# Performance work log

Measured on AMD Instinct MI355X. Metric: run time of the kernel, lower is better.

## Reference

```python
import jax, jax.numpy as jnp
import numpy as np
from jax import lax

SQRT2 = float(np.sqrt(2.0))  # lrelu def_gain
LRELU_SLOPE = 0.2


def setup_inputs() -> dict:
    key = jax.random.key(0)
    ks = jax.random.split(key, 4)
    N, I, O, WD, H = 16, 256, 512, 512, 64
    return {
        "x": jax.random.normal(ks[0], (N, I, H, H), dtype=jnp.float32),
        "w": jax.random.normal(ks[1], (N, WD), dtype=jnp.float32),
        "affine_w": jax.random.normal(ks[2], (I, WD), dtype=jnp.float32),
        "affine_b": jnp.ones((I,), dtype=jnp.float32),
        "weight": jax.random.normal(ks[3], (O, I, 3, 3), dtype=jnp.float32),
        "bias": jnp.zeros((O,), dtype=jnp.float32),
    }


def reference(x, w, affine_w, affine_b, weight, bias):
    N, I, H, W = x.shape
    O, _, kh, kw = weight.shape
    w_dim = affine_w.shape[1]

    # affine (FullyConnectedLayer, weight_gain = 1/sqrt(w_dim))
    styles = w @ (affine_w.T / np.sqrt(w_dim)) + affine_b  # [N, I]

    # modulate + demodulate -> per-sample weights [N, O, I, kh, kw]
    ww = weight[None] * styles[:, None, :, None, None]
    dcoefs = lax.rsqrt(jnp.sum(ww * ww, axis=(2, 3, 4)) + 1e-8)  # [N, O]
    ww = ww * dcoefs[:, :, None, None, None]

    # resample filter: outer([1,3,3,1])/sum, symmetric so flip is a no-op
    f1 = jnp.array([1.0, 3.0, 3.0, 1.0], dtype=x.dtype)
    f1 = f1 / f1.sum()
    f2 = jnp.outer(f1, f1)  # [4, 4]

    # upfirdn2d: pad by padding + (fw-down+1)//2 = 2 per side, depthwise 4x4
    xp = jnp.pad(x, ((0, 0), (0, 0), (2, 2), (2, 2)))
    fk = jnp.broadcast_to(f2[None, None], (I, 1, 4, 4))
    xf = lax.conv_general_dilated(
        xp, fk, window_strides=(1, 1), padding="VALID",
        feature_group_count=I,
        dimension_numbers=("NCHW", "OIHW", "NCHW"))  # [N, I, H+1, W+1]

    # fused grouped conv, stride 2; flip_weight=False -> flip kernel spatially
    wk = ww[:, :, :, ::-1, ::-1].reshape(N * O, I, kh, kw)
    xg = xf.reshape(1, N * I, xf.shape[2], xf.shape[3])
    y = lax.conv_general_dilated(
        xg, wk, window_strides=(2, 2), padding="VALID",
        feature_group_count=N,
        dimension_numbers=("NCHW", "OIHW", "NCHW"))
    y = y.reshape(N, O, y.shape[2], y.shape[3])  # [N, O, H/2, W/2]

    # bias + lrelu, act_gain = sqrt(2), no clamp
    y = y + bias[None, :, None, None]
    y = jnp.where(y >= 0, y, LRELU_SLOPE * y) * SQRT2
    return y
```

## Files before the change

### kernel.cpp

```cpp
#include <hip/hip_runtime.h>
#include <cstdint>
#include <cstddef>


typedef short bf16x8 __attribute__((ext_vector_type(8)));
typedef float f32x4  __attribute__((ext_vector_type(4)));

#define CGSTR 4460544
#define NSTR  278784
#define PLSTR 69696

__device__ __forceinline__ unsigned short f2bf(float f) {
  union { float f; unsigned u; } v; v.f = f;
  unsigned r = (v.u + 0x7FFFu + ((v.u >> 16) & 1u)) >> 16;
  return (unsigned short)r;
}

__device__ __forceinline__ void gload_lds16(const void* g, void* l) {
  __builtin_amdgcn_global_load_lds((const __attribute__((address_space(1))) void*)g,
                                   (__attribute__((address_space(3))) void*)l,
                                   16, 0, 0);
}

__global__ void styles_kernel(const float* __restrict__ w, const float* __restrict__ aw,
                              const float* __restrict__ ab, float* __restrict__ styles) {
  const int n = blockIdx.x;
  const int i = threadIdx.x;
  const float4* wr = (const float4*)(w + (size_t)n * 512);
  const float4* ar = (const float4*)(aw + (size_t)i * 512);
  float acc = 0.f;
#pragma unroll 4
  for (int k = 0; k < 128; ++k) {
    float4 a = wr[k], c = ar[k];
    acc += a.x * c.x + a.y * c.y + a.z * c.z + a.w * c.w;
  }
  styles[n * 256 + i] = acc * 0.04419417382415922f + ab[i];
}

__global__ void wtcvt_kernel(const float* __restrict__ wt, unsigned short* __restrict__ wtb,
                             float* __restrict__ wsq) {
  const int o = blockIdx.x;
  const int i = threadIdx.x;
  const float* p = wt + ((size_t)o * 256 + i) * 9;
  float v[9];
  float s = 0.f;
#pragma unroll
  for (int k = 0; k < 9; ++k) { v[k] = p[k]; s += v[k] * v[k]; }
  wsq[o * 256 + i] = s;
#pragma unroll
  for (int tap = 0; tap < 9; ++tap)
    wtb[((size_t)tap * 512 + o) * 256 + i] = f2bf(v[8 - tap]);
}

__global__ void dcoefs_kernel(const float* __restrict__ wsq, const float* __restrict__ styles,
                              float* __restrict__ dcoefs) {
  __shared__ float st2[256];
  const int n = blockIdx.x;
  const int t = threadIdx.x;
  if (t < 256) { float s = styles[n * 256 + t]; st2[t] = s * s; }
  __syncthreads();
  const float4* wr = (const float4*)(wsq + (size_t)t * 256);
  const float4* sr = (const float4*)st2;
  float acc = 0.f;
#pragma unroll 4
  for (int k = 0; k < 64; ++k) {
    float4 a = wr[k], c = sr[k];
    acc += a.x * c.x + a.y * c.y + a.z * c.z + a.w * c.w;
  }
  dcoefs[n * 512 + t] = 1.0f / sqrtf(acc + 1e-8f);
}

__global__ __launch_bounds__(256, 4) void blur_kernel(const float* __restrict__ x,
                                                      const float* __restrict__ styles,
                                                      unsigned short* __restrict__ xfp) {
  __shared__ unsigned short shls[2][64][68];
  const int b = blockIdx.x;
  const int n = b >> 6;
  const int rem = b & 63;
  const int rg = rem >> 2;
  const int cg = rem & 3;
  const int tid = threadIdx.x;
  const int ch = tid >> 2;
  const int s4 = tid & 3;
  const int col0 = s4 * 16;
  const float* xin = x + ((size_t)(n * 256 + cg * 64 + ch) << 12);
  const float sv = styles[n * 256 + cg * 64 + ch];
  const float F0s = 0.125f * sv, F1s = 0.375f * sv;
  const float F0 = 0.125f, F1 = 0.375f;
  const int ybase = rg * 4;
  const int ylim = (rg == 15) ? 5 : 4;
  const size_t obase = (size_t)(cg * 16 + n) * 4 * PLSTR;

  float4 rA[4], rB[4], rC[4], rD[4], rN[4];
  auto load4 = [&](int row, float4* dst) {
    if ((unsigned)row < 64u) {
      const float4* p = (const float4*)(xin + row * 64 + col0);
      dst[0] = p[0]; dst[1] = p[1]; dst[2] = p[2]; dst[3] = p[3];
    } else {
      const float4 z = {0.f, 0.f, 0.f, 0.f};
      dst[0] = z; dst[1] = z; dst[2] = z; dst[3] = z;
    }
  };
  load4(ybase - 2, rA); load4(ybase - 1, rB); load4(ybase, rC); load4(ybase + 1, rD);

#pragma unroll 1
  for (int yy = 0; yy < ylim; ++yy) {
    const int y = ybase + yy;
    load4(y + 2, rN);
    float ve[20];
#pragma unroll
    for (int q = 0; q < 4; ++q) {
      ve[2 + q * 4 + 0] = F0s * rA[q].x + F1s * rB[q].x + F1s * rC[q].x + F0s * rD[q].x;
      ve[2 + q * 4 + 1] = F0s * rA[q].y + F1s * rB[q].y + F1s * rC[q].y + F0s * rD[q].y;
      ve[2 + q * 4 + 2] = F0s * rA[q].z + F1s * rB[q].z + F1s * rC[q].z + F0s * rD[q].z;
      ve[2 + q * 4 + 3] = F0s * rA[q].w + F1s * rB[q].w + F1s * rC[q].w + F0s * rD[q].w;
    }
    float vm2 = __shfl_up(ve[16], 1);
    float vm1 = __shfl_up(ve[17], 1);
    float vp1 = __shfl_down(ve[2], 1);
    if (s4 == 0) { vm2 = 0.f; vm1 = 0.f; }
    if (s4 == 3) vp1 = 0.f;
    ve[0] = vm2; ve[1] = vm1; ve[18] = vp1; ve[19] = 0.f;
    unsigned short hv[17];
#pragma unroll
    for (int pl = 0; pl < 17; ++pl)
      hv[pl] = f2bf(F0 * ve[pl] + F1 * ve[pl + 1] + F1 * ve[pl + 2] + F0 * ve[pl + 3]);
    unsigned short (*sh)[68] = shls[yy & 1];
    unsigned* dst32 = (unsigned*)&sh[ch][col0];
#pragma unroll
    for (int q = 0; q < 8; ++q)
      dst32[q] = (unsigned)hv[2 * q] | ((unsigned)hv[2 * q + 1] << 16);
    if (s4 == 3) sh[ch][64] = hv[16];
    __syncthreads();
    const int ph = y & 1, r = y >> 1;
#pragma unroll 1
    for (int sI = tid; sI < 520; sI += 256) {
      const int p = sI >> 3, j = sI & 7;
      union { bf16x8 vv; unsigned short u[8]; } pk;
#pragma unroll
      for (int k = 0; k < 8; ++k) pk.u[k] = sh[j * 8 + k][p];
      const int pw = p & 1, cc = p >> 1;
      const size_t off = obase + (size_t)(ph * 2 + pw) * PLSTR + (r * 33 + cc) * 64 + j * 8;
      *(bf16x8*)(xfp + off) = pk.vv;
    }
#pragma unroll
    for (int q = 0; q < 4; ++q) { rA[q] = rB[q]; rB[q] = rC[q]; rC[q] = rD[q]; rD[q] = rN[q]; }
  }
}

__global__ __launch_bounds__(256) void conv_kernel(
    const unsigned short* __restrict__ wtb,
    const unsigned short* __restrict__ xfp,
    const float* __restrict__ dcoefs,
    const float* __restrict__ bias,
    float* __restrict__ out) {
  __shared__ unsigned short As0[4096], As1[4096];
  __shared__ unsigned short Bs0[4096], Bs1[4096];
  const int idx = blockIdx.x;
  const int om = idx >> 7;
  const int g = idx & 127;
  const int pt = g >> 4;
  const int n = g & 15;
  const int o0 = om << 7;
  const int oh0 = pt << 2;
  const int tid = threadIdx.x;
  const int lane = tid & 63;
  const int wv = tid >> 6;
  const int wm = wv >> 1;
  const int wp = wv & 1;
  const int ml = lane & 15;
  const int kq = lane >> 4;

  f32x4 acc[4][4];
  const f32x4 zz = {0.f, 0.f, 0.f, 0.f};
#pragma unroll
  for (int i = 0; i < 4; ++i)
#pragma unroll
    for (int j = 0; j < 4; ++j) acc[i][j] = zz;

  const int s0 = wv * 128 + lane, s1 = s0 + 64;
  const int r0 = s0 >> 2, g0 = (s0 & 3) * 8;
  const int r1 = s1 >> 2, g1 = (s1 & 3) * 8;
  const int aoff0 = (o0 + r0) * 256 + g0;
  const int aoff1 = (o0 + r1) * 256 + g1;
  const int row0 = oh0 + (r0 >> 5), col0 = r0 & 31;
  const int row1 = oh0 + (r1 >> 5), col1 = r1 & 31;
  const size_t nB = (size_t)n * NSTR;

  auto stage = [&](int kt, unsigned short* As, unsigned short* Bs) {
    const int tap = kt >> 3, kb = kt & 7;
    const int kh = (tap * 11) >> 5;
    const int kw = tap - kh * 3;
    const int ph = kh & 1, dr = kh >> 1;
    const int pw = kw & 1, dc = kw >> 1;
    const unsigned short* At = wtb + tap * 131072 + kb * 32;
    gload_lds16(At + aoff0, As + wv * 1024);
    gload_lds16(At + aoff1, As + wv * 1024 + 512);
    const unsigned short* Bt = xfp + (size_t)(kb >> 1) * CGSTR + nB +
                               (size_t)(ph * 2 + pw) * PLSTR + (kb & 1) * 32;
    gload_lds16(Bt + ((row0 + dr) * 33 + col0 + dc) * 64 + g0, Bs + wv * 1024);
    gload_lds16(Bt + ((row1 + dr) * 33 + col1 + dc) * 64 + g1, Bs + wv * 1024 + 512);
  };
  auto compute = [&](const unsigned short* As, const unsigned short* Bs) {
    bf16x8 af[4], bfv[4];
    const bf16x8* A8 = (const bf16x8*)As;
    const bf16x8* B8 = (const bf16x8*)Bs;
#pragma unroll
    for (int t = 0; t < 4; ++t) {
      af[t]  = A8[(wm * 64 + t * 16 + ml) * 4 + kq];
      bfv[t] = B8[(wp * 64 + t * 16 + ml) * 4 + kq];
    }
#pragma unroll
    for (int mt = 0; mt < 4; ++mt)
#pragma unroll
      for (int nt = 0; nt < 4; ++nt)
        acc[mt][nt] = __builtin_amdgcn_mfma_f32_16x16x32_bf16(af[mt], bfv[nt], acc[mt][nt], 0, 0, 0);
  };

  stage(0, As0, Bs0);
#pragma unroll 1
  for (int kt = 0; kt < 72; kt += 2) {
    __syncthreads();
    stage(kt + 1, As1, Bs1);
    compute(As0, Bs0);
    __syncthreads();
    if (kt + 2 < 72) stage(kt + 2, As0, Bs0);
    compute(As1, Bs1);
  }

  f32x4 dc4[4], bi4[4];
#pragma unroll
  for (int mt = 0; mt < 4; ++mt) {
    const int ob = o0 + wm * 64 + mt * 16 + kq * 4;
    dc4[mt] = *(const f32x4*)(dcoefs + n * 512 + ob);
    bi4[mt] = *(const f32x4*)(bias + ob);
  }
#pragma unroll
  for (int mt = 0; mt < 4; ++mt) {
#pragma unroll
    for (int nt = 0; nt < 4; ++nt) {
      const int p = wp * 64 + nt * 16 + ml;
      const int oh = oh0 + (p >> 5), ow = p & 31;
#pragma unroll
      for (int r = 0; r < 4; ++r) {
        const int o = o0 + wm * 64 + mt * 16 + kq * 4 + r;
        float v = acc[mt][nt][r] * dc4[mt][r] + bi4[mt][r];
        v = (v >= 0.f ? v : 0.2f * v) * 1.41421356237309515f;
        out[(((size_t)n * 512 + o) * 32 + oh) * 32 + ow] = v;
      }
    }
  }
}

extern "C" void kernel_launch(void* const* d_in, const int* in_sizes, int n_in,
                              void* d_out, int out_size, void* d_ws, size_t ws_size,
                              hipStream_t stream) {
  const float* x  = (const float*)d_in[0];
  const float* w  = (const float*)d_in[1];
  const float* aw = (const float*)d_in[2];
  const float* ab = (const float*)d_in[3];
  const float* wt = (const float*)d_in[4];
  const float* bs = (const float*)d_in[5];
  float* out = (float*)d_out;

  char* ws = (char*)d_ws;
  float* styles        = (float*)(ws);
  float* dcoefs        = (float*)(ws + 16384);
  float* wsq           = (float*)(ws + 49152);
  unsigned short* wtb  = (unsigned short*)(ws + 573440);
  unsigned short* xfp  = (unsigned short*)(ws + 2932736);

  styles_kernel<<<dim3(16),   dim3(256), 0, stream>>>(w, aw, ab, styles);
  wtcvt_kernel <<<dim3(512),  dim3(256), 0, stream>>>(wt, wtb, wsq);
  dcoefs_kernel<<<dim3(16),   dim3(512), 0, stream>>>(wsq, styles, dcoefs);
  blur_kernel  <<<dim3(1024), dim3(256), 0, stream>>>(x, styles, xfp);
  conv_kernel  <<<dim3(512),  dim3(256), 0, stream>>>(wtb, xfp, dcoefs, bs, out);
}
```

Before: 211.2 us.

## Load conv weight fragments directly to registers; double blur rows per block

In the conv kernel the A operand (weights) is no longer staged through LDS. Each wave now loads its MFMA fragments straight from global memory into registers, double-buffered across k-steps, which removes the A LDS traffic and halves the shared memory footprint. The blur kernel handles 8 output rows per block instead of 4 with half the blocks, cutting the halo-row reloads. The cost is that waves in the same block re-read the same weight rows from global/L2, and register pressure rises.

```diff
diff --git a/kernel.cpp b/kernel.cpp
--- a/kernel.cpp
+++ b/kernel.cpp
@@ -75,8 +75,8 @@
                                                       unsigned short* __restrict__ xfp) {
   __shared__ unsigned short shls[2][64][68];
   const int b = blockIdx.x;
-  const int n = b >> 6;
-  const int rem = b & 63;
+  const int n = b >> 5;
+  const int rem = b & 31;
   const int rg = rem >> 2;
   const int cg = rem & 3;
   const int tid = threadIdx.x;
@@ -87,8 +87,8 @@
   const float sv = styles[n * 256 + cg * 64 + ch];
   const float F0s = 0.125f * sv, F1s = 0.375f * sv;
   const float F0 = 0.125f, F1 = 0.375f;
-  const int ybase = rg * 4;
-  const int ylim = (rg == 15) ? 5 : 4;
+  const int ybase = rg * 8;
+  const int ylim = (rg == 7) ? 9 : 8;
   const size_t obase = (size_t)(cg * 16 + n) * 4 * PLSTR;
 
   float4 rA[4], rB[4], rC[4], rD[4], rN[4];
@@ -154,7 +154,6 @@
     const float* __restrict__ dcoefs,
     const float* __restrict__ bias,
     float* __restrict__ out) {
-  __shared__ unsigned short As0[4096], As1[4096];
   __shared__ unsigned short Bs0[4096], Bs1[4096];
   const int idx = blockIdx.x;
   const int om = idx >> 7;
@@ -181,35 +180,38 @@
   const int s0 = wv * 128 + lane, s1 = s0 + 64;
   const int r0 = s0 >> 2, g0 = (s0 & 3) * 8;
   const int r1 = s1 >> 2, g1 = (s1 & 3) * 8;
-  const int aoff0 = (o0 + r0) * 256 + g0;
-  const int aoff1 = (o0 + r1) * 256 + g1;
   const int row0 = oh0 + (r0 >> 5), col0 = r0 & 31;
   const int row1 = oh0 + (r1 >> 5), col1 = r1 & 31;
   const size_t nB = (size_t)n * NSTR;
 
-  auto stage = [&](int kt, unsigned short* As, unsigned short* Bs) {
+  const unsigned short* aptr[4];
+#pragma unroll
+  for (int t = 0; t < 4; ++t)
+    aptr[t] = wtb + (size_t)(o0 + wm * 64 + t * 16 + ml) * 256 + kq * 8;
+
+  auto stageB = [&](int kt, unsigned short* Bs) {
     const int tap = kt >> 3, kb = kt & 7;
     const int kh = (tap * 11) >> 5;
     const int kw = tap - kh * 3;
     const int ph = kh & 1, dr = kh >> 1;
     const int pw = kw & 1, dc = kw >> 1;
-    const unsigned short* At = wtb + tap * 131072 + kb * 32;
-    gload_lds16(At + aoff0, As + wv * 1024);
-    gload_lds16(At + aoff1, As + wv * 1024 + 512);
     const unsigned short* Bt = xfp + (size_t)(kb >> 1) * CGSTR + nB +
                                (size_t)(ph * 2 + pw) * PLSTR + (kb & 1) * 32;
     gload_lds16(Bt + ((row0 + dr) * 33 + col0 + dc) * 64 + g0, Bs + wv * 1024);
     gload_lds16(Bt + ((row1 + dr) * 33 + col1 + dc) * 64 + g1, Bs + wv * 1024 + 512);
   };
-  auto compute = [&](const unsigned short* As, const unsigned short* Bs) {
-    bf16x8 af[4], bfv[4];
-    const bf16x8* A8 = (const bf16x8*)As;
+  auto loadA = [&](int kt, bf16x8* af) {
+    const int tap = kt >> 3, kb = kt & 7;
+    const int koff = tap * 131072 + kb * 32;
+#pragma unroll
+    for (int t = 0; t < 4; ++t) af[t] = *(const bf16x8*)(aptr[t] + koff);
+  };
+  auto compute = [&](const bf16x8* af, const unsigned short* Bs) {
+    bf16x8 bfv[4];
     const bf16x8* B8 = (const bf16x8*)Bs;
 #pragma unroll
-    for (int t = 0; t < 4; ++t) {
-      af[t]  = A8[(wm * 64 + t * 16 + ml) * 4 + kq];
+    for (int t = 0; t < 4; ++t)
       bfv[t] = B8[(wp * 64 + t * 16 + ml) * 4 + kq];
-    }
 #pragma unroll
     for (int mt = 0; mt < 4; ++mt)
 #pragma unroll
@@ -217,15 +219,18 @@
         acc[mt][nt] = __builtin_amdgcn_mfma_f32_16x16x32_bf16(af[mt], bfv[nt], acc[mt][nt], 0, 0, 0);
   };
 
-  stage(0, As0, Bs0);
+  bf16x8 afA[4], afB[4];
+  stageB(0, Bs0);
+  loadA(0, afA);
 #pragma unroll 1
   for (int kt = 0; kt < 72; kt += 2) {
     __syncthreads();
-    stage(kt + 1, As1, Bs1);
-    compute(As0, Bs0);
+    stageB(kt + 1, Bs1);
+    loadA(kt + 1, afB);
+    compute(afA, Bs0);
     __syncthreads();
-    if (kt + 2 < 72) stage(kt + 2, As0, Bs0);
-    compute(As1, Bs1);
+    if (kt + 2 < 72) { stageB(kt + 2, Bs0); loadA(kt + 2, afA); }
+    compute(afB, Bs1);
   }
 
   f32x4 dc4[4], bi4[4];
@@ -273,6 +278,6 @@
   styles_kernel<<<dim3(16),   dim3(256), 0, stream>>>(w, aw, ab, styles);
   wtcvt_kernel <<<dim3(512),  dim3(256), 0, stream>>>(wt, wtb, wsq);
   dcoefs_kernel<<<dim3(16),   dim3(512), 0, stream>>>(wsq, styles, dcoefs);
-  blur_kernel  <<<dim3(1024), dim3(256), 0, stream>>>(x, styles, xfp);
+  blur_kernel  <<<dim3(512),  dim3(256), 0, stream>>>(x, styles, xfp);
   conv_kernel  <<<dim3(512),  dim3(256), 0, stream>>>(wtb, xfp, dcoefs, bs, out);
 }
```

After: 252.1 us. 19.4% more time.

## Double conv K-tile to 64 with XOR-swizzled LDS and halve blur grid

Applied to the files above, without the earlier changes.

The conv kernel now stages 64-wide K slices (two channel groups per stage), so the main loop runs half as many iterations and needs half as many barriers. Global-to-LDS loads use an XOR swizzle on the 8-element group index, which the fragment reads undo, to avoid LDS bank conflicts. The blur kernel processes 8 output rows per block instead of 4, halving its grid and reusing the sliding row window over more rows. LDS use doubles to 64 KB per block, which may lower occupancy.

```diff
diff --git a/kernel.cpp b/kernel.cpp
--- a/kernel.cpp
+++ b/kernel.cpp
@@ -75,8 +75,8 @@
                                                       unsigned short* __restrict__ xfp) {
   __shared__ unsigned short shls[2][64][68];
   const int b = blockIdx.x;
-  const int n = b >> 6;
-  const int rem = b & 63;
+  const int n = b >> 5;
+  const int rem = b & 31;
   const int rg = rem >> 2;
   const int cg = rem & 3;
   const int tid = threadIdx.x;
@@ -87,8 +87,8 @@
   const float sv = styles[n * 256 + cg * 64 + ch];
   const float F0s = 0.125f * sv, F1s = 0.375f * sv;
   const float F0 = 0.125f, F1 = 0.375f;
-  const int ybase = rg * 4;
-  const int ylim = (rg == 15) ? 5 : 4;
+  const int ybase = rg * 8;
+  const int ylim = (rg == 7) ? 9 : 8;
   const size_t obase = (size_t)(cg * 16 + n) * 4 * PLSTR;
 
   float4 rA[4], rB[4], rC[4], rD[4], rN[4];
@@ -154,8 +154,8 @@
     const float* __restrict__ dcoefs,
     const float* __restrict__ bias,
     float* __restrict__ out) {
-  __shared__ unsigned short As0[4096], As1[4096];
-  __shared__ unsigned short Bs0[4096], Bs1[4096];
+  __shared__ unsigned short As0[8192], Bs0[8192];
+  __shared__ unsigned short As1[8192], Bs1[8192];
   const int idx = blockIdx.x;
   const int om = idx >> 7;
   const int g = idx & 127;
@@ -178,53 +178,62 @@
 #pragma unroll
     for (int j = 0; j < 4; ++j) acc[i][j] = zz;
 
-  const int s0 = wv * 128 + lane, s1 = s0 + 64;
-  const int r0 = s0 >> 2, g0 = (s0 & 3) * 8;
-  const int r1 = s1 >> 2, g1 = (s1 & 3) * 8;
-  const int aoff0 = (o0 + r0) * 256 + g0;
-  const int aoff1 = (o0 + r1) * 256 + g1;
-  const int row0 = oh0 + (r0 >> 5), col0 = r0 & 31;
-  const int row1 = oh0 + (r1 >> 5), col1 = r1 & 31;
+  const int rowbase = wv * 32 + (lane >> 3);
+  const int glog8 = (((lane & 7) ^ ((lane >> 3) & 7))) * 8;
+  int aoffj[4], boffj[4];
+#pragma unroll
+  for (int j = 0; j < 4; ++j) {
+    const int r = rowbase + j * 8;
+    aoffj[j] = (o0 + r) * 256 + glog8;
+    boffj[j] = ((oh0 + (r >> 5)) * 33 + (r & 31)) * 64 + glog8;
+  }
   const size_t nB = (size_t)n * NSTR;
+  const int gi0 = (0 * 4 + kq) ^ (ml & 7);
+  const int gi1 = (1 * 4 + kq) ^ (ml & 7);
 
   auto stage = [&](int kt, unsigned short* As, unsigned short* Bs) {
-    const int tap = kt >> 3, kb = kt & 7;
+    const int tap = kt >> 2, pair = kt & 3;
     const int kh = (tap * 11) >> 5;
     const int kw = tap - kh * 3;
     const int ph = kh & 1, dr = kh >> 1;
     const int pw = kw & 1, dc = kw >> 1;
-    const unsigned short* At = wtb + tap * 131072 + kb * 32;
-    gload_lds16(At + aoff0, As + wv * 1024);
-    gload_lds16(At + aoff1, As + wv * 1024 + 512);
-    const unsigned short* Bt = xfp + (size_t)(kb >> 1) * CGSTR + nB +
-                               (size_t)(ph * 2 + pw) * PLSTR + (kb & 1) * 32;
-    gload_lds16(Bt + ((row0 + dr) * 33 + col0 + dc) * 64 + g0, Bs + wv * 1024);
-    gload_lds16(Bt + ((row1 + dr) * 33 + col1 + dc) * 64 + g1, Bs + wv * 1024 + 512);
+    const unsigned short* At = wtb + tap * 131072 + pair * 64;
+    const unsigned short* Bt = xfp + (size_t)pair * CGSTR + nB +
+                               (size_t)(ph * 2 + pw) * PLSTR + (dr * 33 + dc) * 64;
+#pragma unroll
+    for (int j = 0; j < 4; ++j) {
+      gload_lds16(At + aoffj[j], As + (wv * 256 + j * 64) * 8);
+      gload_lds16(Bt + boffj[j], Bs + (wv * 256 + j * 64) * 8);
+    }
   };
   auto compute = [&](const unsigned short* As, const unsigned short* Bs) {
-    bf16x8 af[4], bfv[4];
     const bf16x8* A8 = (const bf16x8*)As;
     const bf16x8* B8 = (const bf16x8*)Bs;
 #pragma unroll
-    for (int t = 0; t < 4; ++t) {
-      af[t]  = A8[(wm * 64 + t * 16 + ml) * 4 + kq];
-      bfv[t] = B8[(wp * 64 + t * 16 + ml) * 4 + kq];
-    }
-#pragma unroll
-    for (int mt = 0; mt < 4; ++mt)
-#pragma unroll
-      for (int nt = 0; nt < 4; ++nt)
-        acc[mt][nt] = __builtin_amdgcn_mfma_f32_16x16x32_bf16(af[mt], bfv[nt], acc[mt][nt], 0, 0, 0);
+    for (int h = 0; h < 2; ++h) {
+      const int gi = h ? gi1 : gi0;
+      bf16x8 af[4], bfv[4];
+#pragma unroll
+      for (int t = 0; t < 4; ++t) {
+        af[t]  = A8[(wm * 64 + t * 16 + ml) * 8 + gi];
+        bfv[t] = B8[(wp * 64 + t * 16 + ml) * 8 + gi];
+      }
+#pragma unroll
+      for (int mt = 0; mt < 4; ++mt)
+#pragma unroll
+        for (int nt = 0; nt < 4; ++nt)
+          acc[mt][nt] = __builtin_amdgcn_mfma_f32_16x16x32_bf16(af[mt], bfv[nt], acc[mt][nt], 0, 0, 0);
+    }
   };
 
   stage(0, As0, Bs0);
 #pragma unroll 1
-  for (int kt = 0; kt < 72; kt += 2) {
+  for (int kt = 0; kt < 36; kt += 2) {
     __syncthreads();
     stage(kt + 1, As1, Bs1);
     compute(As0, Bs0);
     __syncthreads();
-    if (kt + 2 < 72) stage(kt + 2, As0, Bs0);
+    if (kt + 2 < 36) stage(kt + 2, As0, Bs0);
     compute(As1, Bs1);
   }
 
@@ -273,6 +282,6 @@
   styles_kernel<<<dim3(16),   dim3(256), 0, stream>>>(w, aw, ab, styles);
   wtcvt_kernel <<<dim3(512),  dim3(256), 0, stream>>>(wt, wtb, wsq);
   dcoefs_kernel<<<dim3(16),   dim3(512), 0, stream>>>(wsq, styles, dcoefs);
-  blur_kernel  <<<dim3(1024), dim3(256), 0, stream>>>(x, styles, xfp);
+  blur_kernel  <<<dim3(512),  dim3(256), 0, stream>>>(x, styles, xfp);
   conv_kernel  <<<dim3(512),  dim3(256), 0, stream>>>(wtb, xfp, dcoefs, bs, out);
 }
```

New measurement: 197.1 us. 6.7% less time.
